# Performance work log

Measured on AMD Instinct MI355X. Metric: run time of the kernel, lower is better.

## Reference

```python
import jax, jax.numpy as jnp
import numpy as np
from jax import lax


def setup_inputs() -> dict:
    key = jax.random.key(0)
    k1, k2, k3 = jax.random.split(key, 3)
    B, L, T = 1024, 512, 64
    logits = jax.random.normal(k1, (B, L, T), dtype=jnp.float32)
    tags = jax.random.randint(k2, (B, L), 0, T, dtype=jnp.int64)
    mask = jnp.ones((B, L), dtype=jnp.int32)
    trans_m = jax.random.normal(k3, (T, T), dtype=jnp.float32)
    return {"logits": logits, "tags": tags, "mask": mask, "trans_m": trans_m}


def _normalizer(logits_t, mask_t, trans):
    # logits_t: [L, B, T], mask_t: [L, B] float, trans: [T, T]
    alpha0 = logits_t[0]  # [B, T]

    def step(alpha, xs):
        emit, m = xs  # emit [B, T], m [B]
        # alpha[b, i] + trans[i, j] + emit[b, j] -> logsumexp over i
        tmp = alpha[:, :, None] + emit[:, None, :] + trans[None, :, :]  # [B, T, T]
        new_alpha = jax.nn.logsumexp(tmp, axis=1)  # [B, T]
        alpha = jnp.where(m[:, None] > 0, new_alpha, alpha)
        return alpha, None

    alpha, _ = lax.scan(step, alpha0, (logits_t[1:], mask_t[1:]))
    return jax.nn.logsumexp(alpha, axis=1)  # [B]


def _gold_score(logits_t, tags_t, mask_t, trans):
    # logits_t: [L, B, T], tags_t: [L, B] int, mask_t: [L, B] float
    # transition score between consecutive gold tags, masked where next pos is pad
    trans_score = trans[tags_t[:-1], tags_t[1:]] * mask_t[1:]  # [L-1, B]
    # emission score at gold tags, masked at pad positions
    emit = jnp.take_along_axis(logits_t, tags_t[:, :, None], axis=2)[:, :, 0] * mask_t  # [L, B]
    score = (trans_score + emit[:-1]).sum(axis=0) + emit[-1] * mask_t[-1]  # [B]
    return score


def reference(logits, tags, mask, trans_m):
    # forward: feats [B, L, T] -> transpose to [L, B, T]; loss = logZ - gold_score
    logits_t = jnp.transpose(logits, (1, 0, 2)).astype(jnp.float32)  # [L, B, T]
    tags_t = jnp.transpose(tags, (1, 0))  # [L, B]
    mask_t = jnp.transpose(mask, (1, 0)).astype(logits.dtype)  # [L, B]
    all_path = _normalizer(logits_t, mask_t, trans_m)
    gold = _gold_score(logits_t, tags_t, mask_t, trans_m)
    return all_path - gold  # [B] per-sample negative log-likelihood
```

## Files before the change

### kernel.cpp

```cpp
#include <hip/hip_runtime.h>
#include <math.h>


#define TDIM 64
typedef _Float16 f16;
typedef _Float16 f16x2 __attribute__((ext_vector_type(2)));
typedef _Float16 f16x8 __attribute__((ext_vector_type(8)));
typedef float    f32x4 __attribute__((ext_vector_type(4)));
typedef float    fv4   __attribute__((ext_vector_type(4)));

union B8 { f16x8 v; f16x2 p[4]; };

#define MFMA16(A, B, C) __builtin_amdgcn_mfma_f32_16x16x32_f16((A), (B), (C), 0, 0, 0)

typedef __attribute__((address_space(3))) char       lds_char;
typedef __attribute__((address_space(3))) const fv4  lds_cfv4;
typedef __attribute__((address_space(1))) const char g1_char;

#define PLANE_STRIDE 1024
#define SLOT_STRIDE  4096
#define BUF_STRIDE   32768
#define WV_STRIDE    65536
#define BITMAP_OFF   131072
#define SMEM_BYTES   132096

__device__ __forceinline__ f16x2 pk2(float a, float b) {
    f16x2 r; r[0] = (f16)a; r[1] = (f16)b; return r;
}

__device__ __forceinline__ void stage_slot(const float* pp, char* slotbase) {
    __builtin_amdgcn_global_load_lds((g1_char*)(pp + 0),  (lds_char*)(slotbase + 0*PLANE_STRIDE), 16, 0, 0);
    __builtin_amdgcn_global_load_lds((g1_char*)(pp + 4),  (lds_char*)(slotbase + 1*PLANE_STRIDE), 16, 0, 0);
    __builtin_amdgcn_global_load_lds((g1_char*)(pp + 32), (lds_char*)(slotbase + 2*PLANE_STRIDE), 16, 0, 0);
    __builtin_amdgcn_global_load_lds((g1_char*)(pp + 36), (lds_char*)(slotbase + 3*PLANE_STRIDE), 16, 0, 0);
}

template <int DIR>
__device__ __forceinline__ void run_chain(
    const float* __restrict__ logits0,
    const int*   __restrict__ mask0,
    const float* __restrict__ trans,
    char* smem, int w, int l, int L, bool masked,
    float a[16], int& kacc)
{
    const int ml = l & 15;
    const int gl = l >> 4;
    const int H  = L >> 1;

    f16x8 Af[4][2];
    #pragma unroll
    for (int c = 0; c < 4; ++c) {
        const int mlog = 32*(c>>1) + 8*(ml>>2) + 4*(c&1) + (ml&3);
        #pragma unroll
        for (int kc = 0; kc < 2; ++kc) {
            B8 t;
            #pragma unroll
            for (int e = 0; e < 8; e += 2) {
                const int k0 = 32*kc + 8*gl + e;
                float x0, x1;
                if (DIR == 0) { x0 = trans[k0*TDIM + mlog];  x1 = trans[(k0+1)*TDIM + mlog]; }
                else          { x0 = trans[mlog*TDIM + k0];  x1 = trans[mlog*TDIM + k0 + 1]; }
                t.p[e>>1] = pk2(__expf(x0), __expf(x1));
            }
            Af[c][kc] = t.v;
        }
    }

    unsigned* mwv = (unsigned*)(smem + BITMAP_OFF + w * 512);
    const int t0m = DIR ? H : 0;
    const int WPB = H >> 5;
    if (masked) {
        for (int flat = l; flat < 16 * WPB; flat += 64) {
            const int mb = flat / WPB, w8 = flat - mb * WPB;
            unsigned word = 0;
            const int* mp = mask0 + (size_t)mb * L + t0m + 32 * w8;
            for (int j = 0; j < 32; ++j) word |= (mp[j] > 0 ? 1u : 0u) << j;
            mwv[flat] = word;
        }
    }

    #pragma unroll
    for (int i = 0; i < 16; ++i) a[i] = 1.f;
    kacc = 0;

    char* stg = smem + w * WV_STRIDE;
    char* rb0 = stg + 16 * l;
    const float* pp = logits0 + ((size_t)ml * L + (DIR ? (L - 1) : 0)) * TDIM + 8 * gl;
    const int drow = DIR ? -TDIM : TDIM;

    __builtin_amdgcn_sched_barrier(0);

    #pragma unroll
    for (int cpre = 0; cpre < 2; ++cpre) {
        char* cb = stg + cpre * BUF_STRIDE;
        #pragma unroll
        for (int u = 0; u < 8; ++u) {
            stage_slot(pp, cb + u * SLOT_STRIDE);
            pp += drow;
        }
    }

    float Xn[16], Xc[16];
    fv4 q[4];
    const int NSS = H >> 3;
    for (int S = 0; S < NSS; ++S) {
        char* crb = rb0 + (S & 1) * BUF_STRIDE;
        char* cwb = stg + (S & 1) * BUF_STRIDE;

        asm volatile("s_waitcnt vmcnt(32)" ::: "memory");
        __builtin_amdgcn_sched_barrier(0);

        q[0] = *(lds_cfv4*)(crb + 0 * PLANE_STRIDE);
        q[1] = *(lds_cfv4*)(crb + 1 * PLANE_STRIDE);
        q[2] = *(lds_cfv4*)(crb + 2 * PLANE_STRIDE);
        q[3] = *(lds_cfv4*)(crb + 3 * PLANE_STRIDE);
        #pragma unroll
        for (int c = 0; c < 4; ++c) {
            #pragma unroll
            for (int r = 0; r < 4; ++r) Xn[c*4 + r] = __expf(q[c][r]);
        }

        #pragma unroll
        for (int u = 0; u < 8; ++u) {
            #pragma unroll
            for (int i = 0; i < 16; ++i) Xc[i] = Xn[i];
            const int st = 8 * S + u;

            if (u < 7) {
                q[0] = *(lds_cfv4*)(crb + (u+1)*SLOT_STRIDE + 0*PLANE_STRIDE);
                q[1] = *(lds_cfv4*)(crb + (u+1)*SLOT_STRIDE + 1*PLANE_STRIDE);
                q[2] = *(lds_cfv4*)(crb + (u+1)*SLOT_STRIDE + 2*PLANE_STRIDE);
                q[3] = *(lds_cfv4*)(crb + (u+1)*SLOT_STRIDE + 3*PLANE_STRIDE);
            }

            float cand[16];
            if (DIR == 0 && st == 0) {
                #pragma unroll
                for (int i = 0; i < 16; ++i) cand[i] = Xc[i];
            } else {
                float bsrc[16];
                #pragma unroll
                for (int i = 0; i < 16; ++i) bsrc[i] = (DIR == 0) ? a[i] : a[i] * Xc[i];
                B8 b0, b1;
                #pragma unroll
                for (int h = 0; h < 4; ++h) {
                    b0.p[h] = pk2(bsrc[2*h],     bsrc[2*h+1]);
                    b1.p[h] = pk2(bsrc[8 + 2*h], bsrc[8 + 2*h+1]);
                }
                f32x4 D0 = {0.f,0.f,0.f,0.f}, D1 = {0.f,0.f,0.f,0.f};
                f32x4 D2 = {0.f,0.f,0.f,0.f}, D3 = {0.f,0.f,0.f,0.f};
                D0 = MFMA16(Af[0][0], b0.v, D0); D0 = MFMA16(Af[0][1], b1.v, D0);
                D1 = MFMA16(Af[1][0], b0.v, D1); D1 = MFMA16(Af[1][1], b1.v, D1);
                D2 = MFMA16(Af[2][0], b0.v, D2); D2 = MFMA16(Af[2][1], b1.v, D2);
                D3 = MFMA16(Af[3][0], b0.v, D3); D3 = MFMA16(Af[3][1], b1.v, D3);
                if (DIR == 0) {
                    #pragma unroll
                    for (int r = 0; r < 4; ++r) {
                        cand[r]      = D0[r] * Xc[r];
                        cand[4 + r]  = D1[r] * Xc[4 + r];
                        cand[8 + r]  = D2[r] * Xc[8 + r];
                        cand[12 + r] = D3[r] * Xc[12 + r];
                    }
                } else {
                    #pragma unroll
                    for (int r = 0; r < 4; ++r) {
                        cand[r] = D0[r]; cand[4+r] = D1[r];
                        cand[8+r] = D2[r]; cand[12+r] = D3[r];
                    }
                }
                if (masked) {
                    const int dt = DIR ? (H - 1 - st) : st;
                    const unsigned wd = mwv[ml * WPB + (dt >> 5)];
                    const int mb = (wd >> (dt & 31)) & 1;
                    #pragma unroll
                    for (int i = 0; i < 16; ++i) cand[i] = mb ? cand[i] : a[i];
                }
            }

            if (u < 7) {
                #pragma unroll
                for (int c = 0; c < 4; ++c) {
                    #pragma unroll
                    for (int r = 0; r < 4; ++r) Xn[c*4 + r] = __expf(q[c][r]);
                }
            }

            {
                const float ref = __shfl(cand[0], ml);
                const int eb = (__float_as_int(ref) >> 23) & 255;
                kacc += eb - 117;
                const float s = __int_as_float((unsigned)(244 - eb) << 23);
                #pragma unroll
                for (int i = 0; i < 16; ++i) a[i] = cand[i] * s;
            }
        }

        #pragma unroll
        for (int u = 0; u < 8; ++u) {
            stage_slot(pp, cwb + u * SLOT_STRIDE);
            pp += drow;
        }
    }

    asm volatile("s_waitcnt vmcnt(0)" ::: "memory");
}

__global__ __launch_bounds__(256, 1) void crf_mfma_kernel(
    const float* __restrict__ logits,
    const int*   __restrict__ tags,
    const int*   __restrict__ mask,
    const float* __restrict__ trans,
    float* __restrict__ out,
    int L)
{
    const int tid = threadIdx.x;
    const int w   = tid >> 6;
    const int l   = tid & 63;
    const int ml  = l & 15;
    const int gl  = l >> 4;
    const int bg  = blockIdx.x * 16;
    const int bi  = bg + ml;
    const int H   = L >> 1;

    __shared__ __align__(16) char smem[SMEM_BYTES];

    const float* logits0 = logits + (size_t)bg * L * TDIM;
    const int*   mask0   = mask + (size_t)bg * L;

    float a[16];
    int   kacc = 0;
    float gs   = 0.f;

    if (w >= 2) {
        const int t0 = (w - 2) * H;
        const int*   tb  = tags + (size_t)bi * L;
        const int*   mb  = mask + (size_t)bi * L;
        const float* lbg = logits + (size_t)bi * L * TDIM;
        #pragma unroll 4
        for (int i = 0; i < (L >> 3); ++i) {
            const int t  = t0 + gl + 4 * i;
            const int tg = tb[t];
            const float mk = (float)mb[t];
            const float em = lbg[(size_t)t * TDIM + tg];
            const float tr = (t > 0) ? trans[tb[t-1] * TDIM + tg] : 0.f;
            gs += mk * (em + tr);
        }
        gs += __shfl_xor(gs, 16);
        gs += __shfl_xor(gs, 32);
    } else {
        const int t0d = (w == 0) ? 0 : H;
        bool ok = true;
        {
            const int4* m4 = (const int4*)(mask0 + (size_t)ml * L + t0d);
            #pragma unroll 4
            for (int i = 0; i < (H >> 4); ++i) {
                const int4 v = m4[gl * (H >> 4) + i];
                ok = ok && (v.x > 0) && (v.y > 0) && (v.z > 0) && (v.w > 0);
            }
        }
        const bool masked = !__all(ok ? 1 : 0);
        if (w == 0) run_chain<0>(logits0, mask0, trans, smem, w, l, L, masked, a, kacc);
        else        run_chain<1>(logits0, mask0, trans, smem, w, l, L, masked, a, kacc);
    }

    __syncthreads();

    float* zfin = (float*)smem;
    float (*gpart2)[16] = (float(*)[16])(smem + 4096);
    int*   kbuf = (int*)(smem + 4224);

    if (w == 1) {
        #pragma unroll
        for (int i = 0; i < 16; ++i) zfin[l * 16 + i] = a[i];
        if (l < 16) kbuf[l] = kacc;
    }
    if (w >= 2 && l < 16) gpart2[w - 2][l] = gs;

    __syncthreads();

    if (w == 0) {
        float prod = 0.f;
        #pragma unroll
        for (int i = 0; i < 16; ++i) prod += a[i] * zfin[l * 16 + i];
        prod += __shfl_xor(prod, 16);
        prod += __shfl_xor(prod, 32);
        if (l < 16) {
            const float logZ = (float)(kacc + kbuf[l]) * 0.6931471805599453f
                             + __logf(prod);
            out[bg + l] = logZ - (gpart2[0][l] + gpart2[1][l]);
        }
    }
}

extern "C" void kernel_launch(void* const* d_in, const int* in_sizes, int n_in,
                              void* d_out, int out_size, void* d_ws, size_t ws_size,
                              hipStream_t stream) {
    const float* logits = (const float*)d_in[0];
    const int*   tags   = (const int*)d_in[1];
    const int*   mask   = (const int*)d_in[2];
    const float* trans  = (const float*)d_in[3];
    float* out = (float*)d_out;

    const int B = out_size;
    const int L = in_sizes[1] / B;

    crf_mfma_kernel<<<B / 16, 256, 0, stream>>>(logits, tags, mask, trans, out, L);
}
```

Before: 272.1 us.

## Split waves into logits producers with exp and serial chain consumers

```diff
diff --git a/kernel.cpp b/kernel.cpp
--- a/kernel.cpp
+++ b/kernel.cpp
@@ -13,39 +13,80 @@
 
 #define MFMA16(A, B, C) __builtin_amdgcn_mfma_f32_16x16x32_f16((A), (B), (C), 0, 0, 0)
 
-typedef __attribute__((address_space(3))) char       lds_char;
-typedef __attribute__((address_space(3))) const fv4  lds_cfv4;
-typedef __attribute__((address_space(1))) const char g1_char;
-
-#define PLANE_STRIDE 1024
-#define SLOT_STRIDE  4096
-#define BUF_STRIDE   32768
-#define WV_STRIDE    65536
-#define BITMAP_OFF   131072
-#define SMEM_BYTES   132096
-
-__device__ __forceinline__ f16x2 pk2(float a, float b) {
-    f16x2 r; r[0] = (f16)a; r[1] = (f16)b; return r;
-}
-
-__device__ __forceinline__ void stage_slot(const float* pp, char* slotbase) {
-    __builtin_amdgcn_global_load_lds((g1_char*)(pp + 0),  (lds_char*)(slotbase + 0*PLANE_STRIDE), 16, 0, 0);
-    __builtin_amdgcn_global_load_lds((g1_char*)(pp + 4),  (lds_char*)(slotbase + 1*PLANE_STRIDE), 16, 0, 0);
-    __builtin_amdgcn_global_load_lds((g1_char*)(pp + 32), (lds_char*)(slotbase + 2*PLANE_STRIDE), 16, 0, 0);
-    __builtin_amdgcn_global_load_lds((g1_char*)(pp + 36), (lds_char*)(slotbase + 3*PLANE_STRIDE), 16, 0, 0);
+typedef __attribute__((address_space(3))) fv4       lds_fv4;
+typedef __attribute__((address_space(3))) const fv4 lds_cfv4;
+
+#define PLANE      1024
+#define SLOT       4096
+#define BUFSZ      32768
+#define DIRSZ      65536
+#define BITMAP_OFF 131072
+#define SMEM_BYTES 132096
+
+__device__ __forceinline__ f16x2 pkrtz(float a, float b) {
+    return __builtin_bit_cast(f16x2, __builtin_amdgcn_cvt_pkrtz(a, b));
+}
+
+__device__ __forceinline__ void sync_barrier() {
+    asm volatile("s_waitcnt lgkmcnt(0)" ::: "memory");
+    __builtin_amdgcn_s_barrier();
+}
+
+__device__ __forceinline__ const float* produce_one(
+    char* cb, const float* pp, int drow, int lo)
+{
+    fv4 R[8][4];
+    const float* p = pp;
+    #pragma unroll
+    for (int u = 0; u < 8; ++u) {
+        R[u][0] = *(const fv4*)(p + 0);
+        R[u][1] = *(const fv4*)(p + 4);
+        R[u][2] = *(const fv4*)(p + 32);
+        R[u][3] = *(const fv4*)(p + 36);
+        p += drow;
+    }
+    __builtin_amdgcn_sched_barrier(0);
+    #pragma unroll
+    for (int u = 0; u < 8; ++u) {
+        #pragma unroll
+        for (int c = 0; c < 4; ++c) {
+            fv4 x;
+            #pragma unroll
+            for (int r = 0; r < 4; ++r) x[r] = __expf(R[u][c][r]);
+            *(lds_fv4*)(void*)(cb + u * SLOT + c * PLANE + lo) = x;
+        }
+    }
+    return p;
 }
 
 template <int DIR>
-__device__ __forceinline__ void run_chain(
-    const float* __restrict__ logits0,
-    const int*   __restrict__ mask0,
-    const float* __restrict__ trans,
-    char* smem, int w, int l, int L, bool masked,
+__device__ __forceinline__ void produce(char* smem, const float* logits0,
+                                        int l, int L)
+{
+    const int ml = l & 15, gl = l >> 4;
+    const int H = L >> 1;
+    char* base = smem + DIR * DIRSZ;
+    const int lo = 16 * l;
+    const float* pp = logits0 + ((size_t)ml * L + (DIR ? (L - 1) : 0)) * TDIM + 8 * gl;
+    const int drow = DIR ? -TDIM : TDIM;
+    const int NSS = H >> 3;
+
+    pp = produce_one(base, pp, drow, lo);
+    for (int S = 0; S < NSS; ++S) {
+        sync_barrier();
+        if (S + 1 < NSS)
+            pp = produce_one(base + ((S + 1) & 1) * BUFSZ, pp, drow, lo);
+    }
+}
+
+template <int DIR>
+__device__ __forceinline__ void consume(
+    char* smem, const float* __restrict__ trans,
+    const int* __restrict__ mask0, int l, int L, bool masked,
     float a[16], int& kacc)
 {
-    const int ml = l & 15;
-    const int gl = l >> 4;
-    const int H  = L >> 1;
+    const int ml = l & 15, gl = l >> 4;
+    const int H = L >> 1;
 
     f16x8 Af[4][2];
     #pragma unroll
@@ -60,13 +101,14 @@
                 float x0, x1;
                 if (DIR == 0) { x0 = trans[k0*TDIM + mlog];  x1 = trans[(k0+1)*TDIM + mlog]; }
                 else          { x0 = trans[mlog*TDIM + k0];  x1 = trans[mlog*TDIM + k0 + 1]; }
-                t.p[e>>1] = pk2(__expf(x0), __expf(x1));
+                f16x2 h; h[0] = (f16)__expf(x0); h[1] = (f16)__expf(x1);
+                t.p[e>>1] = h;
             }
             Af[c][kc] = t.v;
         }
     }
 
-    unsigned* mwv = (unsigned*)(smem + BITMAP_OFF + w * 512);
+    unsigned* mwv = (unsigned*)(smem + BITMAP_OFF + DIR * 512);
     const int t0m = DIR ? H : 0;
     const int WPB = H >> 5;
     if (masked) {
@@ -82,70 +124,53 @@
     #pragma unroll
     for (int i = 0; i < 16; ++i) a[i] = 1.f;
     kacc = 0;
-
-    char* stg = smem + w * WV_STRIDE;
-    char* rb0 = stg + 16 * l;
-    const float* pp = logits0 + ((size_t)ml * L + (DIR ? (L - 1) : 0)) * TDIM + 8 * gl;
-    const int drow = DIR ? -TDIM : TDIM;
-
-    __builtin_amdgcn_sched_barrier(0);
-
-    #pragma unroll
-    for (int cpre = 0; cpre < 2; ++cpre) {
-        char* cb = stg + cpre * BUF_STRIDE;
-        #pragma unroll
-        for (int u = 0; u < 8; ++u) {
-            stage_slot(pp, cb + u * SLOT_STRIDE);
-            pp += drow;
-        }
-    }
-
-    float Xn[16], Xc[16];
-    fv4 q[4];
+    int   kp = 0;
+    float sp = 1.f;
+
+    char* base = smem + DIR * DIRSZ;
+    const int lo = 16 * l;
+
+    fv4 qc[4], qn[4];
     const int NSS = H >> 3;
     for (int S = 0; S < NSS; ++S) {
-        char* crb = rb0 + (S & 1) * BUF_STRIDE;
-        char* cwb = stg + (S & 1) * BUF_STRIDE;
-
-        asm volatile("s_waitcnt vmcnt(32)" ::: "memory");
-        __builtin_amdgcn_sched_barrier(0);
-
-        q[0] = *(lds_cfv4*)(crb + 0 * PLANE_STRIDE);
-        q[1] = *(lds_cfv4*)(crb + 1 * PLANE_STRIDE);
-        q[2] = *(lds_cfv4*)(crb + 2 * PLANE_STRIDE);
-        q[3] = *(lds_cfv4*)(crb + 3 * PLANE_STRIDE);
-        #pragma unroll
-        for (int c = 0; c < 4; ++c) {
-            #pragma unroll
-            for (int r = 0; r < 4; ++r) Xn[c*4 + r] = __expf(q[c][r]);
-        }
+        sync_barrier();
+        char* cb = base + (S & 1) * BUFSZ;
+        #pragma unroll
+        for (int c = 0; c < 4; ++c)
+            qc[c] = *(lds_cfv4*)(void*)(cb + c * PLANE + lo);
 
         #pragma unroll
         for (int u = 0; u < 8; ++u) {
-            #pragma unroll
-            for (int i = 0; i < 16; ++i) Xc[i] = Xn[i];
             const int st = 8 * S + u;
-
             if (u < 7) {
-                q[0] = *(lds_cfv4*)(crb + (u+1)*SLOT_STRIDE + 0*PLANE_STRIDE);
-                q[1] = *(lds_cfv4*)(crb + (u+1)*SLOT_STRIDE + 1*PLANE_STRIDE);
-                q[2] = *(lds_cfv4*)(crb + (u+1)*SLOT_STRIDE + 2*PLANE_STRIDE);
-                q[3] = *(lds_cfv4*)(crb + (u+1)*SLOT_STRIDE + 3*PLANE_STRIDE);
+                #pragma unroll
+                for (int c = 0; c < 4; ++c)
+                    qn[c] = *(lds_cfv4*)(void*)(cb + (u+1)*SLOT + c*PLANE + lo);
             }
 
             float cand[16];
-            if (DIR == 0 && st == 0) {
-                #pragma unroll
-                for (int i = 0; i < 16; ++i) cand[i] = Xc[i];
+            bool init = (DIR == 0) && (S == 0) && (u == 0);
+            if (init) {
+                #pragma unroll
+                for (int c = 0; c < 4; ++c)
+                    #pragma unroll
+                    for (int r = 0; r < 4; ++r) cand[4*c + r] = qc[c][r];
             } else {
-                float bsrc[16];
-                #pragma unroll
-                for (int i = 0; i < 16; ++i) bsrc[i] = (DIR == 0) ? a[i] : a[i] * Xc[i];
+                float bs[16];
+                if (DIR == 0) {
+                    #pragma unroll
+                    for (int i = 0; i < 16; ++i) bs[i] = a[i];
+                } else {
+                    #pragma unroll
+                    for (int c = 0; c < 4; ++c)
+                        #pragma unroll
+                        for (int r = 0; r < 4; ++r) bs[4*c + r] = a[4*c + r] * qc[c][r];
+                }
                 B8 b0, b1;
                 #pragma unroll
                 for (int h = 0; h < 4; ++h) {
-                    b0.p[h] = pk2(bsrc[2*h],     bsrc[2*h+1]);
-                    b1.p[h] = pk2(bsrc[8 + 2*h], bsrc[8 + 2*h+1]);
+                    b0.p[h] = pkrtz(bs[2*h],     bs[2*h+1]);
+                    b1.p[h] = pkrtz(bs[8 + 2*h], bs[8 + 2*h+1]);
                 }
                 f32x4 D0 = {0.f,0.f,0.f,0.f}, D1 = {0.f,0.f,0.f,0.f};
                 f32x4 D2 = {0.f,0.f,0.f,0.f}, D3 = {0.f,0.f,0.f,0.f};
@@ -156,53 +181,48 @@
                 if (DIR == 0) {
                     #pragma unroll
                     for (int r = 0; r < 4; ++r) {
-                        cand[r]      = D0[r] * Xc[r];
-                        cand[4 + r]  = D1[r] * Xc[4 + r];
-                        cand[8 + r]  = D2[r] * Xc[8 + r];
-                        cand[12 + r] = D3[r] * Xc[12 + r];
+                        cand[r]      = D0[r] * (qc[0][r] * sp);
+                        cand[4 + r]  = D1[r] * (qc[1][r] * sp);
+                        cand[8 + r]  = D2[r] * (qc[2][r] * sp);
+                        cand[12 + r] = D3[r] * (qc[3][r] * sp);
                     }
                 } else {
                     #pragma unroll
                     for (int r = 0; r < 4; ++r) {
-                        cand[r] = D0[r]; cand[4+r] = D1[r];
-                        cand[8+r] = D2[r]; cand[12+r] = D3[r];
+                        cand[r] = D0[r]*sp; cand[4+r] = D1[r]*sp;
+                        cand[8+r] = D2[r]*sp; cand[12+r] = D3[r]*sp;
                     }
                 }
-                if (masked) {
-                    const int dt = DIR ? (H - 1 - st) : st;
-                    const unsigned wd = mwv[ml * WPB + (dt >> 5)];
-                    const int mb = (wd >> (dt & 31)) & 1;
-                    #pragma unroll
-                    for (int i = 0; i < 16; ++i) cand[i] = mb ? cand[i] : a[i];
-                }
-            }
-
+            }
+
+            if (masked && !init) {
+                const int dt = DIR ? (H - 1 - st) : st;
+                const unsigned wd = mwv[ml * WPB + (dt >> 5)];
+                const int mb = (wd >> (dt & 31)) & 1;
+                #pragma unroll
+                for (int i = 0; i < 16; ++i) cand[i] = mb ? cand[i] : a[i];
+                kacc += mb ? kp : 0;
+            } else {
+                kacc += kp;
+            }
+
+            #pragma unroll
+            for (int i = 0; i < 16; ++i) a[i] = cand[i];
+
+            {
+                const float ref = __shfl(a[0], ml);
+                const int eb = (__float_as_int(ref) >> 23) & 255;
+                const bool zz = (eb == 0);
+                kp = zz ? 0 : (eb - 113);
+                sp = __int_as_float(zz ? 0x3f800000u
+                                       : ((unsigned)(240 - eb) << 23));
+            }
             if (u < 7) {
                 #pragma unroll
-                for (int c = 0; c < 4; ++c) {
-                    #pragma unroll
-                    for (int r = 0; r < 4; ++r) Xn[c*4 + r] = __expf(q[c][r]);
-                }
-            }
-
-            {
-                const float ref = __shfl(cand[0], ml);
-                const int eb = (__float_as_int(ref) >> 23) & 255;
-                kacc += eb - 117;
-                const float s = __int_as_float((unsigned)(244 - eb) << 23);
-                #pragma unroll
-                for (int i = 0; i < 16; ++i) a[i] = cand[i] * s;
-            }
-        }
-
-        #pragma unroll
-        for (int u = 0; u < 8; ++u) {
-            stage_slot(pp, cwb + u * SLOT_STRIDE);
-            pp += drow;
-        }
-    }
-
-    asm volatile("s_waitcnt vmcnt(0)" ::: "memory");
+                for (int c = 0; c < 4; ++c) qc[c] = qn[c];
+            }
+        }
+    }
 }
 
 __global__ __launch_bounds__(256, 1) void crf_mfma_kernel(
@@ -229,25 +249,8 @@
 
     float a[16];
     int   kacc = 0;
-    float gs   = 0.f;
-
-    if (w >= 2) {
-        const int t0 = (w - 2) * H;
-        const int*   tb  = tags + (size_t)bi * L;
-        const int*   mb  = mask + (size_t)bi * L;
-        const float* lbg = logits + (size_t)bi * L * TDIM;
-        #pragma unroll 4
-        for (int i = 0; i < (L >> 3); ++i) {
-            const int t  = t0 + gl + 4 * i;
-            const int tg = tb[t];
-            const float mk = (float)mb[t];
-            const float em = lbg[(size_t)t * TDIM + tg];
-            const float tr = (t > 0) ? trans[tb[t-1] * TDIM + tg] : 0.f;
-            gs += mk * (em + tr);
-        }
-        gs += __shfl_xor(gs, 16);
-        gs += __shfl_xor(gs, 32);
-    } else {
+
+    if (w < 2) {
         const int t0d = (w == 0) ? 0 : H;
         bool ok = true;
         {
@@ -259,22 +262,45 @@
             }
         }
         const bool masked = !__all(ok ? 1 : 0);
-        if (w == 0) run_chain<0>(logits0, mask0, trans, smem, w, l, L, masked, a, kacc);
-        else        run_chain<1>(logits0, mask0, trans, smem, w, l, L, masked, a, kacc);
+        if (w == 0) consume<0>(smem, trans, mask0, l, L, masked, a, kacc);
+        else        consume<1>(smem, trans, mask0, l, L, masked, a, kacc);
+    } else {
+        if (w == 2) produce<0>(smem, logits0, l, L);
+        else        produce<1>(smem, logits0, l, L);
+    }
+
+    float gs = 0.f;
+    {
+        const int Q  = L >> 2;
+        const int t0 = w * Q;
+        const int*   tb  = tags + (size_t)bi * L;
+        const int*   mb  = mask + (size_t)bi * L;
+        const float* lbg = logits + (size_t)bi * L * TDIM;
+        #pragma unroll 4
+        for (int i = 0; i < (Q >> 2); ++i) {
+            const int t  = t0 + gl + 4 * i;
+            const int tg = tb[t];
+            const float mk = (float)mb[t];
+            const float em = lbg[(size_t)t * TDIM + tg];
+            const float tr = (t > 0) ? trans[tb[t-1] * TDIM + tg] : 0.f;
+            gs += mk * (em + tr);
+        }
+        gs += __shfl_xor(gs, 16);
+        gs += __shfl_xor(gs, 32);
     }
 
     __syncthreads();
 
     float* zfin = (float*)smem;
-    float (*gpart2)[16] = (float(*)[16])(smem + 4096);
-    int*   kbuf = (int*)(smem + 4224);
+    float (*gpart4)[16] = (float(*)[16])(smem + 4096);
+    int*   kbuf = (int*)(smem + 4096 + 256);
 
     if (w == 1) {
         #pragma unroll
         for (int i = 0; i < 16; ++i) zfin[l * 16 + i] = a[i];
         if (l < 16) kbuf[l] = kacc;
     }
-    if (w >= 2 && l < 16) gpart2[w - 2][l] = gs;
+    if (l < 16) gpart4[w][l] = gs;
 
     __syncthreads();
 
@@ -287,7 +313,8 @@
         if (l < 16) {
             const float logZ = (float)(kacc + kbuf[l]) * 0.6931471805599453f
                              + __logf(prod);
-            out[bg + l] = logZ - (gpart2[0][l] + gpart2[1][l]);
+            out[bg + l] = logZ - (gpart4[0][l] + gpart4[1][l]
+                                + gpart4[2][l] + gpart4[3][l]);
         }
     }
 }
```

After: 273.7 us. Within noise of the previous version (+0.6%).
